# Kernel tuning notes

Hardware: AMD Instinct MI355X
Metric: run time of the kernel (lower is better)

Reference implementation:

```python
import jax, jax.numpy as jnp
import numpy as np

B, S, H, D = 8, 2048, 16, 64  # batch, seq, heads, head_dim
DM = H * D                    # d_model = 1024
W = 4                         # compression window / stride


def setup_inputs() -> dict:
    key = jax.random.key(0)
    ks = jax.random.split(key, 6)
    return {
        "pre_q": jax.random.normal(ks[0], (B, S, H, D), dtype=jnp.float32),
        "pre_k": jax.random.normal(ks[1], (B, S, H, D), dtype=jnp.float32),
        "pre_v": jax.random.normal(ks[2], (B, S, H, D), dtype=jnp.float32),
        "k_conv_kernel": jax.random.normal(ks[3], (W, D, D), dtype=jnp.float32) * (1.0 / np.sqrt(W * D)),
        "k_conv_bias": jnp.zeros((D,), dtype=jnp.float32),
        "v_conv_kernel": jax.random.normal(ks[4], (W, D, D), dtype=jnp.float32) * (1.0 / np.sqrt(W * D)),
        "v_conv_bias": jnp.zeros((D,), dtype=jnp.float32),
        "output_weights": jax.random.normal(ks[5], (DM, DM), dtype=jnp.float32) * (1.0 / np.sqrt(DM)),
        "compression_window": W,
    }


def _compress(x, kernel, bias, window):
    # x: [B, H, S, D] -> strided valid conv along seq -> [B, H, Sc, D]
    b, h, s, d = x.shape
    x2 = x.reshape(b * h, s, d)  # NWC
    y = jax.lax.conv_general_dilated(
        x2, kernel, window_strides=(window,), padding="VALID",
        dimension_numbers=("NWC", "WIO", "NWC")) + bias
    return y.reshape(b, h, -1, d)


def reference(pre_q, pre_k, pre_v, k_conv_kernel, k_conv_bias,
              v_conv_kernel, v_conv_bias, output_weights, compression_window):
    b, s, h, d = pre_q.shape
    q = jnp.transpose(pre_q, (0, 2, 1, 3))  # [B,H,S,D]
    k = jnp.transpose(pre_k, (0, 2, 1, 3))
    v = jnp.transpose(pre_v, (0, 2, 1, 3))
    kc = _compress(k, k_conv_kernel, k_conv_bias, compression_window)  # [B,H,Sc,D]
    vc = _compress(v, v_conv_kernel, v_conv_bias, compression_window)
    scale = 1.0 / np.sqrt(d).astype(np.float32)
    scores = jnp.einsum("bhsd,bhtd->bhst", q, kc) * scale  # [B,H,S,Sc]
    attn = jax.nn.softmax(scores, axis=-1)
    out = jnp.einsum("bhst,bhtd->bhsd", attn, vc)  # [B,H,S,D]
    out = jnp.transpose(out, (0, 2, 1, 3)).reshape(b, s, h * d)  # [B,S,DM]
    return out @ output_weights  # [B,S,DM]
```

## Files before the change

### kernel.cpp

```cpp
#include <hip/hip_runtime.h>
#include <hip/hip_bf16.h>
#include <math.h>

#define B_   8
#define S_   2048
#define H_   16
#define D_   64
#define DM_  1024
#define W_   4
#define SC_  512

typedef float f32x4 __attribute__((ext_vector_type(4)));
typedef short bf16x8 __attribute__((ext_vector_type(8)));
typedef short bf16x4 __attribute__((ext_vector_type(4)));

static __device__ inline short f2bf(float f) {
    union { float f; unsigned u; } v; v.f = f;
    unsigned r = v.u + 0x7fffu + ((v.u >> 16) & 1u);
    return (short)(r >> 16);
}

static __device__ inline short bfc(float f) {
    __hip_bfloat16 h = __float2bfloat16(f);
    union { __hip_bfloat16 h; short s; } u; u.h = h; return u.s;
}

static __device__ inline float fexp2(float x) {
    float r; asm("v_exp_f32 %0, %1" : "=v"(r) : "v"(x)); return r;
}

static __device__ inline void gll16(const void* g, void* l) {
    __builtin_amdgcn_global_load_lds(
        (const __attribute__((address_space(1))) unsigned int*)g,
        (__attribute__((address_space(3))) unsigned int*)l, 16, 0, 0);
}

__global__ __launch_bounds__(256) void wprep_kernel(
    const float* __restrict__ Wg, const float* __restrict__ kk,
    const float* __restrict__ vk, short* __restrict__ Wt,
    short* __restrict__ BkT)
{
    __shared__ float ws[64][68];
    const int tid  = threadIdx.x;
    const int bidx = blockIdx.x;

    const float* src; short* dst;
    int k0, scol, sstride, dstride;
    if (bidx < 256) {
        scol = (bidx & 15) * 64; k0 = (bidx >> 4) * 64;
        src = Wg; sstride = 1024;
        dst = Wt + (size_t)scol * 1024; dstride = 1024;
    } else {
        int idx = bidx - 256;
        int which = idx >> 2;
        k0 = (idx & 3) * 64; scol = 0;
        src = which ? vk : kk; sstride = 64;
        dst = BkT + (size_t)which * 64 * 256; dstride = 256;
    }

    #pragma unroll
    for (int i = 0; i < 4; ++i) {
        int idx = i * 256 + tid;
        int row = idx >> 4, c4 = idx & 15;
        float4 v = *(const float4*)(src + (size_t)(k0 + row) * sstride + scol + c4 * 4);
        *(float4*)(&ws[row][c4 * 4]) = v;
    }
    __syncthreads();
    #pragma unroll
    for (int i = 0; i < 2; ++i) {
        int idx = i * 256 + tid;
        int n = idx >> 3, kc8 = idx & 7;
        bf16x8 o;
        #pragma unroll
        for (int j = 0; j < 8; ++j) o[j] = f2bf(ws[kc8 * 8 + j][n]);
        *(bf16x8*)(dst + (size_t)n * dstride + k0 + kc8 * 8) = o;
    }
}

__global__ __launch_bounds__(256) void compress_all(
    const float* __restrict__ xk, const float* __restrict__ xv,
    const short* __restrict__ bkt2,
    const float* __restrict__ kbias, const float* __restrict__ vbias,
    short* __restrict__ yk, short* __restrict__ yv)
{
    __shared__ __align__(16) char Ah[16384];
    __shared__ __align__(16) char Al[16384];
    __shared__ __align__(16) char Bs[32768];
    const int tid   = threadIdx.x;
    const int sel   = blockIdx.x & 1;
    const int inner = blockIdx.x >> 1;
    const int bid   = (inner & 7) * 256 + (inner >> 3);
    const int tile  = bid & 15;
    const int bh    = bid >> 4;
    const int h     = bh & 15;
    const int b     = bh >> 4;
    const int t0    = tile * 32;
    const int s0    = t0 * 4;

    const float* x    = sel ? xv : xk;
    const short* bkt  = bkt2 + sel * 64 * 256;
    const float* bias = sel ? vbias : kbias;

    #pragma unroll
    for (int i = 0; i < 8; ++i) {
        int idx = i * 256 + tid;
        int sl = idx >> 4, c4 = idx & 15;
        float4 v = *(const float4*)(x + (((size_t)(b * S_ + s0 + sl) * H_ + h) * D_) + c4 * 4);
        int tl = sl >> 2, k = (sl & 3) * 64 + c4 * 4;
        bf16x4 h4, l4;
        #pragma unroll
        for (int j = 0; j < 4; ++j) {
            float f = ((const float*)&v)[j];
            short hs = f2bf(f);
            union { unsigned u; float f; } hf; hf.u = ((unsigned)(unsigned short)hs) << 16;
            h4[j] = hs;
            l4[j] = f2bf(f - hf.f);
        }
        int base = (tl * 256 + k) * 2;
        int sw = (tl & 7) << 4;
        *(bf16x4*)(Ah + (base ^ sw)) = h4;
        *(bf16x4*)(Al + (base ^ sw)) = l4;
    }
    #pragma unroll
    for (int i = 0; i < 8; ++i) {
        int idx = i * 256 + tid;
        int dr = idx >> 5, part = idx & 31;
        bf16x8 bv = *(const bf16x8*)(bkt + dr * 256 + part * 8);
        *(bf16x8*)(Bs + ((dr * 512 + part * 16) ^ ((dr & 7) << 4))) = bv;
    }

    const int w = tid >> 6, ln = tid & 63, ln15 = ln & 15, hi = ln >> 4;
    const int wm = w & 1, wn = w >> 1;
    f32x4 acc[2];
    #pragma unroll
    for (int nf = 0; nf < 2; ++nf) {
        float bv = bias[wn * 32 + nf * 16 + ln15];
        acc[nf] = (f32x4){bv, bv, bv, bv};
    }
    __syncthreads();

    const int arow = wm * 16 + ln15;
    const int asw  = (arow & 7) << 4;
    #pragma unroll
    for (int kst = 0; kst < 16; ++kst) {
        const char* Asel = (kst < 8) ? Ah : Al;
        int kb = (kst & 7) * 64 + hi * 16;
        bf16x8 af = *(const bf16x8*)(Asel + ((arow * 512 + kb) ^ asw));
        #pragma unroll
        for (int nf = 0; nf < 2; ++nf) {
            int br = wn * 32 + nf * 16 + ln15;
            bf16x8 b8 = *(const bf16x8*)(Bs + ((br * 512 + kb) ^ ((br & 7) << 4)));
            acc[nf] = __builtin_amdgcn_mfma_f32_16x16x32_bf16(af, b8, acc[nf], 0, 0, 0);
        }
    }

    #pragma unroll
    for (int nf = 0; nf < 2; ++nf) {
        int dout = wn * 32 + nf * 16 + ln15;
        #pragma unroll
        for (int r = 0; r < 4; ++r) {
            float vv = acc[nf][r];
            if (!sel) {
                int t = t0 + wm * 16 + hi * 4 + r;
                yk[((size_t)bh * SC_ + t) * 64 + dout] = f2bf(vv);
            } else {
                int p = r + 4 * wm + 8 * hi;
                yv[((size_t)bh * 64 + dout) * SC_ + t0 + p] = f2bf(vv);
            }
        }
    }
}

__global__ __launch_bounds__(1024) void attn_kernel(
    const float* __restrict__ q,
    const short* __restrict__ kc,
    const short* __restrict__ vct,
    short* __restrict__ xb)
{
    extern __shared__ __align__(16) char smem[];
    char* klds = smem;
    char* vlds = smem + 65536;

    const int tid  = threadIdx.x;
    const int bid  = (blockIdx.x & 7) * 64 + (blockIdx.x >> 3);
    const int qc   = bid & 3;
    const int bh   = bid >> 2;
    const int h    = bh & 15;
    const int b    = bh >> 4;
    const int w    = tid >> 6;
    const int ln   = tid & 63;
    const int ln15 = ln & 15;
    const int hi   = ln >> 4;
    const int sbase = qc * 512 + w * 32;
    const int swz  = (ln15 & 7) << 4;

    const short* kg = kc + (size_t)bh * SC_ * 64;
    const short* vg = vct + (size_t)bh * 64 * SC_;

    #pragma unroll
    for (int i = 0; i < 4; ++i) {
        int idx = i * 1024 + tid;
        int row = idx >> 3, part = idx & 7;
        bf16x8 kv = *(const bf16x8*)(kg + idx * 8);
        *(bf16x8*)(klds + ((row * 128 + part * 16) ^ ((row & 7) << 4))) = kv;
    }
    #pragma unroll
    for (int i = 0; i < 4; ++i) {
        int idx = i * 1024 + tid;
        int row = idx >> 6, part = idx & 63;
        bf16x8 vv = *(const bf16x8*)(vg + idx * 8);
        *(bf16x8*)(vlds + ((row * 1024 + part * 16) ^ ((row & 7) << 4))) = vv;
    }

    bf16x8 qb[2][2];
    {
        const float qs = 0.18033688011112042f;
        #pragma unroll
        for (int qf = 0; qf < 2; ++qf) {
            const float* qrow = q + (((size_t)(b * S_ + sbase + qf * 16 + ln15)) * H_ + h) * D_;
            #pragma unroll
            for (int dblk = 0; dblk < 2; ++dblk) {
                const float* p = qrow + dblk * 32 + hi * 8;
                #pragma unroll
                for (int j = 0; j < 8; ++j) qb[qf][dblk][j] = bfc(p[j] * qs);
            }
        }
    }

    const char* kp0 = klds + ln15 * 128 + ((hi * 16) ^ swz);
    const char* kp1 = klds + ln15 * 128 + ((64 + hi * 16) ^ swz);
    const char* vp0 = vlds + ln15 * 1024 + ((hi * 16) ^ swz);
    const char* vp1 = vlds + ln15 * 1024 + ((64 + hi * 16) ^ swz);

    f32x4 oa0[4], oa1[4];
    #pragma unroll
    for (int ns = 0; ns < 4; ++ns) {
        oa0[ns] = (f32x4){0.f, 0.f, 0.f, 0.f};
        oa1[ns] = (f32x4){0.f, 0.f, 0.f, 0.f};
    }
    float lrun0 = 0.f, lrun1 = 0.f;

    __syncthreads();

    #pragma unroll
    for (int kt = 0; kt < 8; ++kt) {
        f32x4 d0[4], d1[4];
        __builtin_amdgcn_s_setprio(1);
        #pragma unroll
        for (int ks = 0; ks < 4; ++ks) {
            bf16x8 ka0 = *(const bf16x8*)(kp0 + kt * 8192 + ks * 2048);
            bf16x8 ka1 = *(const bf16x8*)(kp1 + kt * 8192 + ks * 2048);
            d0[ks] = __builtin_amdgcn_mfma_f32_16x16x32_bf16(ka0, qb[0][0], (f32x4){0.f,0.f,0.f,0.f}, 0, 0, 0);
            d0[ks] = __builtin_amdgcn_mfma_f32_16x16x32_bf16(ka1, qb[0][1], d0[ks], 0, 0, 0);
            d1[ks] = __builtin_amdgcn_mfma_f32_16x16x32_bf16(ka0, qb[1][0], (f32x4){0.f,0.f,0.f,0.f}, 0, 0, 0);
            d1[ks] = __builtin_amdgcn_mfma_f32_16x16x32_bf16(ka1, qb[1][1], d1[ks], 0, 0, 0);
        }
        __builtin_amdgcn_s_setprio(0);

        bf16x8 pa0[2], pa1[2];
        #pragma unroll
        for (int ks = 0; ks < 4; ++ks)
            #pragma unroll
            for (int r = 0; r < 4; ++r) {
                float e0 = fexp2(d0[ks][r]);
                float e1 = fexp2(d1[ks][r]);
                lrun0 += e0; lrun1 += e1;
                pa0[ks >> 1][(ks & 1) * 4 + r] = bfc(e0);
                pa1[ks >> 1][(ks & 1) * 4 + r] = bfc(e1);
            }

        __builtin_amdgcn_s_setprio(1);
        #pragma unroll
        for (int ns = 0; ns < 4; ++ns) {
            bf16x8 vb0 = *(const bf16x8*)(vp0 + ns * 16384 + kt * 128);
            bf16x8 vb1 = *(const bf16x8*)(vp1 + ns * 16384 + kt * 128);
            oa0[ns] = __builtin_amdgcn_mfma_f32_16x16x32_bf16(pa0[0], vb0, oa0[ns], 0, 0, 0);
            oa0[ns] = __builtin_amdgcn_mfma_f32_16x16x32_bf16(pa0[1], vb1, oa0[ns], 0, 0, 0);
            oa1[ns] = __builtin_amdgcn_mfma_f32_16x16x32_bf16(pa1[0], vb0, oa1[ns], 0, 0, 0);
            oa1[ns] = __builtin_amdgcn_mfma_f32_16x16x32_bf16(pa1[1], vb1, oa1[ns], 0, 0, 0);
        }
        __builtin_amdgcn_s_setprio(0);
    }

    lrun0 += __shfl_xor(lrun0, 16);
    lrun0 += __shfl_xor(lrun0, 32);
    lrun1 += __shfl_xor(lrun1, 16);
    lrun1 += __shfl_xor(lrun1, 32);
    float li0[4], li1[4];
    #pragma unroll
    for (int r = 0; r < 4; ++r) {
        li0[r] = 1.f / __shfl(lrun0, hi * 4 + r);
        li1[r] = 1.f / __shfl(lrun1, hi * 4 + r);
    }
    #pragma unroll
    for (int ns = 0; ns < 4; ++ns)
        #pragma unroll
        for (int r = 0; r < 4; ++r) {
            size_t i0 = ((size_t)(b * S_ + sbase + hi * 4 + r)) * DM_ + h * 64 + ns * 16 + ln15;
            xb[i0] = f2bf(oa0[ns][r] * li0[r]);
            size_t i1 = ((size_t)(b * S_ + sbase + 16 + hi * 4 + r)) * DM_ + h * 64 + ns * 16 + ln15;
            xb[i1] = f2bf(oa1[ns][r] * li1[r]);
        }
}

__global__ __launch_bounds__(256) void proj_kernel(
    const short* __restrict__ Xb,
    const short* __restrict__ Wt,
    float* __restrict__ out)
{
    __shared__ __align__(16) short As0[128 * 64];
    __shared__ __align__(16) short Bs0[128 * 64];
    __shared__ __align__(16) short As1[128 * 64];
    __shared__ __align__(16) short Bs1[128 * 64];
    const int tid  = threadIdx.x;
    const int wid  = tid >> 6;
    const int ln   = tid & 63;
    const int ln15 = ln & 15;
    const int hi   = ln >> 4;
    const int wr   = wid >> 1, wc = wid & 1;
    const int bid  = (blockIdx.x & 7) * 128 + (blockIdx.x >> 3);
    const int tn   = bid & 7, tm = bid >> 3;
    const int m0   = tm * 128, n0 = tn * 128;
    const int spart = tid & 7;

    f32x4 acc[4][4];
    #pragma unroll
    for (int i = 0; i < 4; ++i)
        #pragma unroll
        for (int j = 0; j < 4; ++j) acc[i][j] = (f32x4){0.f, 0.f, 0.f, 0.f};

    auto stage = [&](short* A, short* B, int k0) {
        #pragma unroll
        for (int i = 0; i < 4; ++i) {
            int row = (i * 256 + tid) >> 3;
            int ldsoff = __builtin_amdgcn_readfirstlane((i * 256 + (tid & ~63)) * 16);
            gll16(Xb + (size_t)(m0 + row) * 1024 + k0 + spart * 8, (char*)A + ldsoff);
            gll16(Wt + (size_t)(n0 + row) * 1024 + k0 + spart * 8, (char*)B + ldsoff);
        }
    };
    auto compute = [&](const short* A, const short* B) {
        #pragma unroll
        for (int ks = 0; ks < 2; ++ks) {
            bf16x8 af[4], bfr[4];
            #pragma unroll
            for (int mf = 0; mf < 4; ++mf)
                af[mf] = *(const bf16x8*)((const char*)A + (wr * 64 + mf * 16 + ln15) * 128 + ks * 64 + hi * 16);
            #pragma unroll
            for (int nf = 0; nf < 4; ++nf)
                bfr[nf] = *(const bf16x8*)((const char*)B + (wc * 64 + nf * 16 + ln15) * 128 + ks * 64 + hi * 16);
            #pragma unroll
            for (int mf = 0; mf < 4; ++mf)
                #pragma unroll
                for (int nf = 0; nf < 4; ++nf)
                    acc[mf][nf] = __builtin_amdgcn_mfma_f32_16x16x32_bf16(af[mf], bfr[nf], acc[mf][nf], 0, 0, 0);
        }
    };

    stage(As0, Bs0, 0);
    __syncthreads();

    #pragma unroll
    for (int k0 = 0; k0 < 1024; k0 += 128) {
        stage(As1, Bs1, k0 + 64);
        compute(As0, Bs0);
        __syncthreads();
        if (k0 + 128 < 1024)
            stage(As0, Bs0, k0 + 128);
        compute(As1, Bs1);
        __syncthreads();
    }

    #pragma unroll
    for (int mf = 0; mf < 4; ++mf)
        #pragma unroll
        for (int nf = 0; nf < 4; ++nf)
            #pragma unroll
            for (int r = 0; r < 4; ++r)
                out[(size_t)(m0 + wr * 64 + mf * 16 + hi * 4 + r) * 1024 + n0 + wc * 64 + nf * 16 + ln15] =
                    acc[mf][nf][r];
}

extern "C" void kernel_launch(void* const* d_in, const int* in_sizes, int n_in,
                              void* d_out, int out_size, void* d_ws, size_t ws_size,
                              hipStream_t stream) {
    const float* pre_q = (const float*)d_in[0];
    const float* pre_k = (const float*)d_in[1];
    const float* pre_v = (const float*)d_in[2];
    const float* kkern = (const float*)d_in[3];
    const float* kbias = (const float*)d_in[4];
    const float* vkern = (const float*)d_in[5];
    const float* vbias = (const float*)d_in[6];
    const float* wout  = (const float*)d_in[7];
    float* out = (float*)d_out;

    short* Xb  = (short*)d_ws;
    short* kcb = Xb + (size_t)(B_ * S_) * DM_;
    short* vct = kcb + (size_t)B_ * H_ * SC_ * D_;
    short* Wtb = vct + (size_t)B_ * H_ * SC_ * D_;
    short* BkT = Wtb + (size_t)DM_ * DM_;

    wprep_kernel<<<264, 256, 0, stream>>>(wout, kkern, vkern, Wtb, BkT);
    compress_all<<<2 * B_ * H_ * 16, 256, 0, stream>>>(pre_k, pre_v, BkT, kbias, vbias, kcb, vct);
    attn_kernel<<<B_ * H_ * (S_ / 512), 1024, 131072, stream>>>(pre_q, kcb, vct, Xb);
    proj_kernel<<<DM_ / 128 * ((B_ * S_) / 128), 256, 0, stream>>>(Xb, Wtb, out);
}
```

Measured before the change: 154.5 us.

## Shrink attention blocks to 128 queries and stream K/V through LDS in two halves

The attention kernel now launches 512-thread blocks, each covering 128 query rows with 16 rows per wave, instead of 1024-thread blocks covering 512 rows. Only half of K/V is kept in LDS at a time (64 KB static instead of 128 KB dynamic), loaded in two phases with a barrier between them. V fragments are also loaded ahead of the score MFMAs. The aim is higher occupancy (several blocks per CU) and more blocks in flight. The trade-off is that each K/V tile is reloaded from global/L2 four times as often, there is less MFMA work per wave to hide latency, and each block adds a barrier.

```diff
diff --git a/kernel.cpp b/kernel.cpp
--- a/kernel.cpp
+++ b/kernel.cpp
@@ -171,135 +171,124 @@
     }
 }
 
-__global__ __launch_bounds__(1024) void attn_kernel(
+__global__ __launch_bounds__(512) void attn_kernel(
     const float* __restrict__ q,
     const short* __restrict__ kc,
     const short* __restrict__ vct,
     short* __restrict__ xb)
 {
-    extern __shared__ __align__(16) char smem[];
-    char* klds = smem;
-    char* vlds = smem + 65536;
+    __shared__ __align__(16) char klds[32768];
+    __shared__ __align__(16) char vlds[32768];
 
     const int tid  = threadIdx.x;
-    const int bid  = (blockIdx.x & 7) * 64 + (blockIdx.x >> 3);
-    const int qc   = bid & 3;
-    const int bh   = bid >> 2;
+    const int bid  = (blockIdx.x & 7) * 256 + (blockIdx.x >> 3);
+    const int qc   = bid & 15;
+    const int bh   = bid >> 4;
     const int h    = bh & 15;
     const int b    = bh >> 4;
     const int w    = tid >> 6;
     const int ln   = tid & 63;
     const int ln15 = ln & 15;
     const int hi   = ln >> 4;
-    const int sbase = qc * 512 + w * 32;
+    const int sbase = qc * 128 + w * 16;
     const int swz  = (ln15 & 7) << 4;
 
     const short* kg = kc + (size_t)bh * SC_ * 64;
     const short* vg = vct + (size_t)bh * 64 * SC_;
 
-    #pragma unroll
-    for (int i = 0; i < 4; ++i) {
-        int idx = i * 1024 + tid;
-        int row = idx >> 3, part = idx & 7;
-        bf16x8 kv = *(const bf16x8*)(kg + idx * 8);
-        *(bf16x8*)(klds + ((row * 128 + part * 16) ^ ((row & 7) << 4))) = kv;
-    }
-    #pragma unroll
-    for (int i = 0; i < 4; ++i) {
-        int idx = i * 1024 + tid;
-        int row = idx >> 6, part = idx & 63;
-        bf16x8 vv = *(const bf16x8*)(vg + idx * 8);
-        *(bf16x8*)(vlds + ((row * 1024 + part * 16) ^ ((row & 7) << 4))) = vv;
-    }
-
-    bf16x8 qb[2][2];
+    const int krow = tid >> 3, kpart = tid & 7;
+    const int vrow = tid >> 5, vpart = tid & 31;
+
+    bf16x8 qb[2];
     {
         const float qs = 0.18033688011112042f;
-        #pragma unroll
-        for (int qf = 0; qf < 2; ++qf) {
-            const float* qrow = q + (((size_t)(b * S_ + sbase + qf * 16 + ln15)) * H_ + h) * D_;
-            #pragma unroll
-            for (int dblk = 0; dblk < 2; ++dblk) {
-                const float* p = qrow + dblk * 32 + hi * 8;
-                #pragma unroll
-                for (int j = 0; j < 8; ++j) qb[qf][dblk][j] = bfc(p[j] * qs);
-            }
+        const float* qrow = q + (((size_t)(b * S_ + sbase + ln15)) * H_ + h) * D_;
+        #pragma unroll
+        for (int dblk = 0; dblk < 2; ++dblk) {
+            const float* p = qrow + dblk * 32 + hi * 8;
+            #pragma unroll
+            for (int j = 0; j < 8; ++j) qb[dblk][j] = bfc(p[j] * qs);
         }
     }
 
     const char* kp0 = klds + ln15 * 128 + ((hi * 16) ^ swz);
     const char* kp1 = klds + ln15 * 128 + ((64 + hi * 16) ^ swz);
-    const char* vp0 = vlds + ln15 * 1024 + ((hi * 16) ^ swz);
-    const char* vp1 = vlds + ln15 * 1024 + ((64 + hi * 16) ^ swz);
-
-    f32x4 oa0[4], oa1[4];
-    #pragma unroll
-    for (int ns = 0; ns < 4; ++ns) {
-        oa0[ns] = (f32x4){0.f, 0.f, 0.f, 0.f};
-        oa1[ns] = (f32x4){0.f, 0.f, 0.f, 0.f};
-    }
-    float lrun0 = 0.f, lrun1 = 0.f;
-
-    __syncthreads();
-
-    #pragma unroll
-    for (int kt = 0; kt < 8; ++kt) {
-        f32x4 d0[4], d1[4];
-        __builtin_amdgcn_s_setprio(1);
-        #pragma unroll
-        for (int ks = 0; ks < 4; ++ks) {
-            bf16x8 ka0 = *(const bf16x8*)(kp0 + kt * 8192 + ks * 2048);
-            bf16x8 ka1 = *(const bf16x8*)(kp1 + kt * 8192 + ks * 2048);
-            d0[ks] = __builtin_amdgcn_mfma_f32_16x16x32_bf16(ka0, qb[0][0], (f32x4){0.f,0.f,0.f,0.f}, 0, 0, 0);
-            d0[ks] = __builtin_amdgcn_mfma_f32_16x16x32_bf16(ka1, qb[0][1], d0[ks], 0, 0, 0);
-            d1[ks] = __builtin_amdgcn_mfma_f32_16x16x32_bf16(ka0, qb[1][0], (f32x4){0.f,0.f,0.f,0.f}, 0, 0, 0);
-            d1[ks] = __builtin_amdgcn_mfma_f32_16x16x32_bf16(ka1, qb[1][1], d1[ks], 0, 0, 0);
-        }
-        __builtin_amdgcn_s_setprio(0);
-
-        bf16x8 pa0[2], pa1[2];
-        #pragma unroll
-        for (int ks = 0; ks < 4; ++ks)
-            #pragma unroll
-            for (int r = 0; r < 4; ++r) {
-                float e0 = fexp2(d0[ks][r]);
-                float e1 = fexp2(d1[ks][r]);
-                lrun0 += e0; lrun1 += e1;
-                pa0[ks >> 1][(ks & 1) * 4 + r] = bfc(e0);
-                pa1[ks >> 1][(ks & 1) * 4 + r] = bfc(e1);
+    const char* vp0 = vlds + ln15 * 512 + ((hi * 16) ^ swz);
+    const char* vp1 = vlds + ln15 * 512 + ((64 + hi * 16) ^ swz);
+
+    f32x4 oa[4];
+    #pragma unroll
+    for (int ns = 0; ns < 4; ++ns) oa[ns] = (f32x4){0.f, 0.f, 0.f, 0.f};
+    float lrun = 0.f;
+
+    #pragma unroll
+    for (int ph = 0; ph < 2; ++ph) {
+        if (ph) __syncthreads();
+        #pragma unroll
+        for (int i = 0; i < 4; ++i) {
+            int row = krow + i * 64;
+            bf16x8 kv = *(const bf16x8*)(kg + (ph * 256 + row) * 64 + kpart * 8);
+            *(bf16x8*)(klds + ((row * 128 + kpart * 16) ^ ((row & 7) << 4))) = kv;
+        }
+        #pragma unroll
+        for (int i = 0; i < 4; ++i) {
+            int row = vrow + i * 16;
+            bf16x8 vv = *(const bf16x8*)(vg + (size_t)row * SC_ + ph * 256 + vpart * 8);
+            *(bf16x8*)(vlds + ((row * 512 + vpart * 16) ^ ((row & 7) << 4))) = vv;
+        }
+        __syncthreads();
+
+        #pragma unroll
+        for (int kt = 0; kt < 4; ++kt) {
+            bf16x8 vb0[4], vb1[4];
+            #pragma unroll
+            for (int ns = 0; ns < 4; ++ns) {
+                vb0[ns] = *(const bf16x8*)(vp0 + ns * 8192 + kt * 128);
+                vb1[ns] = *(const bf16x8*)(vp1 + ns * 8192 + kt * 128);
             }
 
-        __builtin_amdgcn_s_setprio(1);
-        #pragma unroll
-        for (int ns = 0; ns < 4; ++ns) {
-            bf16x8 vb0 = *(const bf16x8*)(vp0 + ns * 16384 + kt * 128);
-            bf16x8 vb1 = *(const bf16x8*)(vp1 + ns * 16384 + kt * 128);
-            oa0[ns] = __builtin_amdgcn_mfma_f32_16x16x32_bf16(pa0[0], vb0, oa0[ns], 0, 0, 0);
-            oa0[ns] = __builtin_amdgcn_mfma_f32_16x16x32_bf16(pa0[1], vb1, oa0[ns], 0, 0, 0);
-            oa1[ns] = __builtin_amdgcn_mfma_f32_16x16x32_bf16(pa1[0], vb0, oa1[ns], 0, 0, 0);
-            oa1[ns] = __builtin_amdgcn_mfma_f32_16x16x32_bf16(pa1[1], vb1, oa1[ns], 0, 0, 0);
-        }
-        __builtin_amdgcn_s_setprio(0);
-    }
-
-    lrun0 += __shfl_xor(lrun0, 16);
-    lrun0 += __shfl_xor(lrun0, 32);
-    lrun1 += __shfl_xor(lrun1, 16);
-    lrun1 += __shfl_xor(lrun1, 32);
-    float li0[4], li1[4];
-    #pragma unroll
-    for (int r = 0; r < 4; ++r) {
-        li0[r] = 1.f / __shfl(lrun0, hi * 4 + r);
-        li1[r] = 1.f / __shfl(lrun1, hi * 4 + r);
-    }
+            f32x4 d[4];
+            __builtin_amdgcn_s_setprio(1);
+            #pragma unroll
+            for (int ks = 0; ks < 4; ++ks) {
+                bf16x8 ka0 = *(const bf16x8*)(kp0 + kt * 8192 + ks * 2048);
+                bf16x8 ka1 = *(const bf16x8*)(kp1 + kt * 8192 + ks * 2048);
+                d[ks] = __builtin_amdgcn_mfma_f32_16x16x32_bf16(ka0, qb[0], (f32x4){0.f,0.f,0.f,0.f}, 0, 0, 0);
+                d[ks] = __builtin_amdgcn_mfma_f32_16x16x32_bf16(ka1, qb[1], d[ks], 0, 0, 0);
+            }
+            __builtin_amdgcn_s_setprio(0);
+
+            bf16x8 pa[2];
+            #pragma unroll
+            for (int ks = 0; ks < 4; ++ks)
+                #pragma unroll
+                for (int r = 0; r < 4; ++r) {
+                    float e = fexp2(d[ks][r]);
+                    lrun += e;
+                    pa[ks >> 1][(ks & 1) * 4 + r] = bfc(e);
+                }
+
+            __builtin_amdgcn_s_setprio(1);
+            #pragma unroll
+            for (int ns = 0; ns < 4; ++ns) {
+                oa[ns] = __builtin_amdgcn_mfma_f32_16x16x32_bf16(pa[0], vb0[ns], oa[ns], 0, 0, 0);
+                oa[ns] = __builtin_amdgcn_mfma_f32_16x16x32_bf16(pa[1], vb1[ns], oa[ns], 0, 0, 0);
+            }
+            __builtin_amdgcn_s_setprio(0);
+        }
+    }
+
+    lrun += __shfl_xor(lrun, 16);
+    lrun += __shfl_xor(lrun, 32);
+    float li[4];
+    #pragma unroll
+    for (int r = 0; r < 4; ++r) li[r] = 1.f / __shfl(lrun, hi * 4 + r);
     #pragma unroll
     for (int ns = 0; ns < 4; ++ns)
         #pragma unroll
         for (int r = 0; r < 4; ++r) {
             size_t i0 = ((size_t)(b * S_ + sbase + hi * 4 + r)) * DM_ + h * 64 + ns * 16 + ln15;
-            xb[i0] = f2bf(oa0[ns][r] * li0[r]);
-            size_t i1 = ((size_t)(b * S_ + sbase + 16 + hi * 4 + r)) * DM_ + h * 64 + ns * 16 + ln15;
-            xb[i1] = f2bf(oa1[ns][r] * li1[r]);
+            xb[i0] = f2bf(oa[ns][r] * li[r]);
         }
 }
 
@@ -401,6 +390,6 @@
 
     wprep_kernel<<<264, 256, 0, stream>>>(wout, kkern, vkern, Wtb, BkT);
     compress_all<<<2 * B_ * H_ * 16, 256, 0, stream>>>(pre_k, pre_v, BkT, kbias, vbias, kcb, vct);
-    attn_kernel<<<B_ * H_ * (S_ / 512), 1024, 131072, stream>>>(pre_q, kcb, vct, Xb);
+    attn_kernel<<<B_ * H_ * (S_ / 128), 512, 0, stream>>>(pre_q, kcb, vct, Xb);
     proj_kernel<<<DM_ / 128 * ((B_ * S_) / 128), 256, 0, stream>>>(Xb, Wtb, out);
 }
```

New measurement: 182.0 us. 1.18x slower.
